# Kernel optimization log

Hardware: AMD Instinct MI355X
Metric: run time of the kernel (lower is better)

## Reference

```python
import jax, jax.numpy as jnp
import numpy as np
import math

D_MODEL = 512
N_HEAD = 8
D_FF = 2048
B, S, S_ENC = 2, 2048, 2048
EPS = 1e-5


def _linear_params(key, d_in, d_out):
    kw, kb = jax.random.split(key)
    w = jax.random.normal(kw, (d_in, d_out), dtype=jnp.float32) * 0.02
    b = jax.random.normal(kb, (d_out,), dtype=jnp.float32) * 0.02
    return w, b


def setup_inputs() -> dict:
    key = jax.random.key(0)
    ks = jax.random.split(key, 16)
    dec = jax.random.normal(ks[0], (B, S, D_MODEL), dtype=jnp.float32)
    enc = jax.random.normal(ks[1], (B, S_ENC, D_MODEL), dtype=jnp.float32)
    src_mask = jnp.ones((B, 1, 1, S_ENC), dtype=jnp.int32)  # no padding
    tgt_mask = jnp.tril(jnp.ones((S, S), dtype=jnp.int32))[None, None]  # causal
    inp = {"dec": dec, "enc": enc, "src_mask": src_mask, "tgt_mask": tgt_mask}
    # self-attention projections
    for i, nm in enumerate(["sa_wq", "sa_wk", "sa_wv", "sa_wo"]):
        w, b = _linear_params(ks[2 + i], D_MODEL, D_MODEL)
        inp[nm], inp[nm.replace("w", "b")] = w, b
    # cross-attention projections
    for i, nm in enumerate(["ca_wq", "ca_wk", "ca_wv", "ca_wo"]):
        w, b = _linear_params(ks[6 + i], D_MODEL, D_MODEL)
        inp[nm], inp[nm.replace("w", "b")] = w, b
    # FFN
    inp["ffn_w1"], inp["ffn_b1"] = _linear_params(ks[10], D_MODEL, D_FF)
    inp["ffn_w2"], inp["ffn_b2"] = _linear_params(ks[11], D_FF, D_MODEL)
    # LayerNorms (gamma=1, beta=0 init as in torch)
    for i in (1, 2, 3):
        inp[f"ln{i}_g"] = jnp.ones((D_MODEL,), dtype=jnp.float32)
        inp[f"ln{i}_b"] = jnp.zeros((D_MODEL,), dtype=jnp.float32)
    return inp


def _layer_norm(x, g, b):
    mu = jnp.mean(x, axis=-1, keepdims=True)
    var = jnp.mean(jnp.square(x - mu), axis=-1, keepdims=True)
    return (x - mu) * jax.lax.rsqrt(var + EPS) * g + b


def _mha(xq, xkv, wq, bq, wk, bk, wv, bv, wo, bo, mask):
    Bq, Sq, D = xq.shape
    Sk = xkv.shape[1]
    d_k = D // N_HEAD
    def split(x, s):
        return x.reshape(x.shape[0], s, N_HEAD, d_k).transpose(0, 2, 1, 3)  # [B,H,S,dk]
    q = split(xq @ wq + bq, Sq)
    k = split(xkv @ wk + bk, Sk)
    v = split(xkv @ wv + bv, Sk)
    scores = jnp.einsum("bhqd,bhkd->bhqk", q, k) / math.sqrt(d_k)
    if mask is not None:
        scores = jnp.where(mask == 0, jnp.float32(-1e9), scores)
    attn = jax.nn.softmax(scores, axis=-1)
    out = jnp.einsum("bhqk,bhkd->bhqd", attn, v)
    out = out.transpose(0, 2, 1, 3).reshape(Bq, Sq, D)
    return out @ wo + bo


def reference(dec, enc, src_mask, tgt_mask,
              sa_wq, sa_bq, sa_wk, sa_bk, sa_wv, sa_bv, sa_wo, sa_bo,
              ca_wq, ca_bq, ca_wk, ca_bk, ca_wv, ca_bv, ca_wo, ca_bo,
              ffn_w1, ffn_b1, ffn_w2, ffn_b2,
              ln1_g, ln1_b, ln2_g, ln2_b, ln3_g, ln3_b):
    # dropout is identity in eval mode
    x = _mha(dec, dec, sa_wq, sa_bq, sa_wk, sa_bk, sa_wv, sa_bv, sa_wo, sa_bo, tgt_mask)
    x = _layer_norm(x + dec, ln1_g, ln1_b)
    _x = x
    x = _mha(x, enc, ca_wq, ca_bq, ca_wk, ca_bk, ca_wv, ca_bv, ca_wo, ca_bo, src_mask)
    x = _layer_norm(x + _x, ln2_g, ln2_b)
    _x = x
    x = jax.nn.relu(x @ ffn_w1 + ffn_b1) @ ffn_w2 + ffn_b2
    x = _layer_norm(x + _x, ln3_g, ln3_b)
    return x
```

## Files before the change

### kernel.cpp

```cpp
#include <hip/hip_runtime.h>


#define D_MODEL 512
#define NHEAD 8
#define DK 64
#define SEQ 2048
#define MTOK 4096
#define DFF 2048

typedef __attribute__((ext_vector_type(8))) short bf16x8;
typedef __attribute__((ext_vector_type(4))) float f32x4;

__device__ __forceinline__ unsigned short f2bf(float x) {
  unsigned u = __float_as_uint(x);
  u += 0x7FFF + ((u >> 16) & 1);
  return (unsigned short)(u >> 16);
}
__device__ __forceinline__ unsigned pack2(float a, float b) {
  return (unsigned)f2bf(a) | ((unsigned)f2bf(b) << 16);
}
__device__ __forceinline__ void load_lds16(const unsigned short* g, unsigned short* l) {
  __builtin_amdgcn_global_load_lds(
      (const __attribute__((address_space(1))) void*)g,
      (__attribute__((address_space(3))) void*)l, 16, 0, 0);
}

struct WDesc { const float* src; unsigned short* dst; int K; int N; };
struct WPack { WDesc d[10]; };

__global__ __launch_bounds__(256)
void wprep_kernel(WPack p) {
  const WDesc wd = p.d[blockIdx.y];
  const int ntx = wd.N >> 5;
  const int ntile = (wd.K >> 5) * ntx;
  if ((int)blockIdx.x >= ntile) return;
  const int n0 = (blockIdx.x % ntx) * 32;
  const int k0 = (blockIdx.x / ntx) * 32;
  __shared__ float T[32][33];
  const int tid = threadIdx.x;
  {
    const int r = tid >> 3, c4 = (tid & 7) * 4;
    float4 v = *(const float4*)(wd.src + (long)(k0 + r) * wd.N + n0 + c4);
    T[r][c4] = v.x; T[r][c4 + 1] = v.y; T[r][c4 + 2] = v.z; T[r][c4 + 3] = v.w;
  }
  __syncthreads();
  {
    const int n = tid >> 3, kq = (tid & 7) * 4;
    ushort4 o;
    o.x = f2bf(T[kq + 0][n]); o.y = f2bf(T[kq + 1][n]);
    o.z = f2bf(T[kq + 2][n]); o.w = f2bf(T[kq + 3][n]);
    *(ushort4*)(wd.dst + (long)(n0 + n) * wd.K + k0 + kq) = o;
  }
}

__global__ __launch_bounds__(256)
void cast_kernel(const float* __restrict__ s, unsigned short* __restrict__ d, int n8) {
  const int i = blockIdx.x * 256 + threadIdx.x;
  if (i >= n8) return;
  float4 a = *(const float4*)(s + (long)i * 8);
  float4 b = *(const float4*)(s + (long)i * 8 + 4);
  uint4 o;
  o.x = pack2(a.x, a.y); o.y = pack2(a.z, a.w);
  o.z = pack2(b.x, b.y); o.w = pack2(b.z, b.w);
  *(uint4*)(d + (long)i * 8) = o;
}

template<int MODE>
__global__ __launch_bounds__(256)
void gemm_bf16(const unsigned short* __restrict__ A, const unsigned short* __restrict__ Wt,
               const float* __restrict__ bias, const float* __restrict__ res,
               void* __restrict__ outp, int M, int N, int K, float scale) {
  __shared__ unsigned short As[4096];
  __shared__ unsigned short Bs[2048];
  const int tid = threadIdx.x;
  const int w = tid >> 6, lane = tid & 63, g = lane >> 4, li = lane & 15;
  const int m0 = blockIdx.x * 128, n0 = blockIdx.y * 64;
  const int wm = w >> 1, wn = w & 1;

  f32x4 acc[4][2] = {};
  const int a0kg = tid >> 7, a0m = tid & 127;
  const int a1kg = (tid + 256) >> 7, a1m = (tid + 256) & 127;
  const int bkg = tid >> 6, bn = tid & 63;
  const unsigned short* Ap0 = A + (long)(m0 + a0m) * K + a0kg * 8;
  const unsigned short* Ap1 = A + (long)(m0 + a1m) * K + a1kg * 8;
  const unsigned short* Bp = Wt + (long)(n0 + bn) * K + bkg * 8;

  for (int k0 = 0; k0 < K; k0 += 32) {
    __syncthreads();
    load_lds16(Ap0 + k0, &As[(w * 64) * 8]);
    load_lds16(Ap1 + k0, &As[(256 + w * 64) * 8]);
    load_lds16(Bp + k0, &Bs[(w * 64) * 8]);
    __syncthreads();
    bf16x8 af[4], bfr[2];
#pragma unroll
    for (int mf = 0; mf < 4; mf++)
      af[mf] = *(const bf16x8*)&As[(g * 128 + wm * 64 + mf * 16 + li) * 8];
#pragma unroll
    for (int nf = 0; nf < 2; nf++)
      bfr[nf] = *(const bf16x8*)&Bs[(g * 64 + wn * 32 + nf * 16 + li) * 8];
#pragma unroll
    for (int mf = 0; mf < 4; mf++)
#pragma unroll
      for (int nf = 0; nf < 2; nf++)
        acc[mf][nf] = __builtin_amdgcn_mfma_f32_16x16x32_bf16(af[mf], bfr[nf], acc[mf][nf], 0, 0, 0);
  }

#pragma unroll
  for (int nf = 0; nf < 2; nf++) {
    const int c = n0 + wn * 32 + nf * 16 + li;
    const float bv = bias[c];
#pragma unroll
    for (int mf = 0; mf < 4; mf++) {
#pragma unroll
      for (int j = 0; j < 4; j++) {
        const int r = m0 + wm * 64 + mf * 16 + g * 4 + j;
        float v = acc[mf][nf][j] + bv;
        if (MODE == 0) {
          v *= scale;
          const int b = r >> 11, s = r & (SEQ - 1), h = c >> 6, d = c & 63;
          ((unsigned short*)outp)[(((long)(b * NHEAD + h)) * SEQ + s) * DK + d] = f2bf(v);
        } else if (MODE == 1) {
          v += res[(long)r * N + c];
          ((float*)outp)[(long)r * N + c] = v;
        } else {
          v = fmaxf(v, 0.f);
          ((unsigned short*)outp)[(long)r * N + c] = f2bf(v);
        }
      }
    }
  }
}

template<bool CAUSAL>
__global__ __launch_bounds__(256)
void attn_bf16(const unsigned short* __restrict__ Qg, const unsigned short* __restrict__ Kg,
               const unsigned short* __restrict__ Vg, unsigned short* __restrict__ Og) {
  __shared__ unsigned short Qp[8192];
  __shared__ unsigned short Kp[4096];
  __shared__ unsigned short Vt[4096];
  __shared__ unsigned short Pl[4][2048];
  const int tid = threadIdx.x;
  const int w = tid >> 6, lane = tid & 63, g = lane >> 4, li = lane & 15;
  const int qb = blockIdx.x, bh = blockIdx.y;
  const int q0 = qb * 128;
  const long base = (long)bh * SEQ * DK;

#pragma unroll
  for (int i = 0; i < 4; i++) {
    const int idx = i * 256 + tid;
    const int dg = idx >> 7, q = idx & 127;
    load_lds16(Qg + base + (long)(q0 + q) * DK + dg * 8, &Qp[(i * 256 + w * 64) * 8]);
  }
  __syncthreads();
  bf16x8 bq[2][2];
#pragma unroll
  for (int qf = 0; qf < 2; qf++)
#pragma unroll
    for (int ks = 0; ks < 2; ks++)
      bq[qf][ks] = *(const bf16x8*)&Qp[((ks * 4 + g) * 128 + w * 32 + qf * 16 + li) * 8];

  f32x4 oacc[2][4] = {};
  float mrun[2] = {-1e30f, -1e30f};
  float denom[2] = {0.f, 0.f};

  const int vdg = tid >> 5;
  const int vs0 = (tid & 31) * 2;
  const int vsg = vs0 >> 3, vso = vs0 & 7;

  const int ntile = CAUSAL ? (2 * qb + 2) : (SEQ / 64);
  for (int t = 0; t < ntile; t++) {
    const int k0 = t * 64;
    __syncthreads();
#pragma unroll
    for (int i = 0; i < 2; i++) {
      const int idx = i * 256 + tid;
      const int dg = idx >> 6, kk = idx & 63;
      load_lds16(Kg + base + (long)(k0 + kk) * DK + dg * 8, &Kp[(i * 256 + w * 64) * 8]);
    }
    {
      const unsigned short* vsrc = Vg + base + (long)(k0 + vs0) * DK + vdg * 8;
      uint4 r0 = *(const uint4*)vsrc;
      uint4 r1 = *(const uint4*)(vsrc + DK);
      unsigned short u0[8], u1[8];
      *(uint4*)u0 = r0; *(uint4*)u1 = r1;
#pragma unroll
      for (int e = 0; e < 8; e++) {
        const int d = vdg * 8 + e;
        const int dsw = d ^ (vsg & 7);
        *(unsigned*)&Vt[(vsg * 64 + dsw) * 8 + vso] =
            (unsigned)u0[e] | ((unsigned)u1[e] << 16);
      }
    }
    __syncthreads();

    f32x4 sacc[4][2] = {};
#pragma unroll
    for (int ks = 0; ks < 2; ks++) {
#pragma unroll
      for (int kf = 0; kf < 4; kf++) {
        bf16x8 ka = *(const bf16x8*)&Kp[((ks * 4 + g) * 64 + kf * 16 + li) * 8];
#pragma unroll
        for (int qf = 0; qf < 2; qf++)
          sacc[kf][qf] = __builtin_amdgcn_mfma_f32_16x16x32_bf16(ka, bq[qf][ks], sacc[kf][qf], 0, 0, 0);
      }
    }
    if (CAUSAL && t >= 2 * qb) {
#pragma unroll
      for (int kf = 0; kf < 4; kf++)
#pragma unroll
        for (int qf = 0; qf < 2; qf++)
#pragma unroll
          for (int j = 0; j < 4; j++) {
            const int kg_ = k0 + kf * 16 + g * 4 + j;
            const int qg_ = q0 + w * 32 + qf * 16 + li;
            if (kg_ > qg_) sacc[kf][qf][j] = -1e30f;
          }
    }
    float corrv[2];
#pragma unroll
    for (int qf = 0; qf < 2; qf++) {
      float mx = -1e30f;
#pragma unroll
      for (int kf = 0; kf < 4; kf++)
#pragma unroll
        for (int j = 0; j < 4; j++) mx = fmaxf(mx, sacc[kf][qf][j]);
      mx = fmaxf(mx, __shfl_xor(mx, 16, 64));
      mx = fmaxf(mx, __shfl_xor(mx, 32, 64));
      const float mn = fmaxf(mrun[qf], mx);
      const float corr = __expf(mrun[qf] - mn);
      mrun[qf] = mn;
      float ps = 0.f;
#pragma unroll
      for (int kf = 0; kf < 4; kf++)
#pragma unroll
        for (int j = 0; j < 4; j++) {
          const float p = __expf(sacc[kf][qf][j] - mn);
          sacc[kf][qf][j] = p;
          ps += p;
        }
      ps += __shfl_xor(ps, 16, 64);
      ps += __shfl_xor(ps, 32, 64);
      denom[qf] = denom[qf] * corr + ps;
      corrv[qf] = corr;
    }
#pragma unroll
    for (int mf = 0; mf < 2; mf++)
#pragma unroll
      for (int j = 0; j < 4; j++) {
        const float cf = __shfl(corrv[mf], g * 4 + j, 64);
#pragma unroll
        for (int df = 0; df < 4; df++) oacc[mf][df][j] *= cf;
      }
#pragma unroll
    for (int kf = 0; kf < 4; kf++)
#pragma unroll
      for (int qf = 0; qf < 2; qf++) {
        uint2 pv;
        pv.x = pack2(sacc[kf][qf][0], sacc[kf][qf][1]);
        pv.y = pack2(sacc[kf][qf][2], sacc[kf][qf][3]);
        *(uint2*)&Pl[w][((kf * 2 + (g >> 1)) * 32 + qf * 16 + li) * 8 + (g & 1) * 4] = pv;
      }
#pragma unroll
    for (int ks2 = 0; ks2 < 2; ks2++) {
      const int sg = ks2 * 4 + g;
#pragma unroll
      for (int mf = 0; mf < 2; mf++) {
        bf16x8 pa = *(const bf16x8*)&Pl[w][(sg * 32 + mf * 16 + li) * 8];
#pragma unroll
        for (int df = 0; df < 4; df++) {
          bf16x8 vb = *(const bf16x8*)&Vt[(sg * 64 + ((df * 16 + li) ^ (sg & 7))) * 8];
          oacc[mf][df] = __builtin_amdgcn_mfma_f32_16x16x32_bf16(pa, vb, oacc[mf][df], 0, 0, 0);
        }
      }
    }
  }

  const int b = bh >> 3, h = bh & 7;
  float rinv[2] = {1.f / denom[0], 1.f / denom[1]};
#pragma unroll
  for (int mf = 0; mf < 2; mf++)
#pragma unroll
    for (int j = 0; j < 4; j++) {
      const float dj = __shfl(rinv[mf], g * 4 + j, 64);
      const int q = q0 + w * 32 + mf * 16 + g * 4 + j;
#pragma unroll
      for (int df = 0; df < 4; df++) {
        const int col = h * DK + df * 16 + li;
        Og[((long)(b * SEQ + q)) * D_MODEL + col] = f2bf(oacc[mf][df][j] * dj);
      }
    }
}

template<bool DUAL>
__global__ __launch_bounds__(256)
void ln_kernel(const float* __restrict__ x, const float* __restrict__ gam,
               const float* __restrict__ bet, float* __restrict__ out,
               unsigned short* __restrict__ outb) {
  const int row = blockIdx.x * 4 + (threadIdx.x >> 6);
  const int lane = threadIdx.x & 63;
  const float* xr = x + (long)row * D_MODEL;
  float4 v0 = *(const float4*)&xr[lane * 8];
  float4 v1 = *(const float4*)&xr[lane * 8 + 4];
  float xv[8] = {v0.x, v0.y, v0.z, v0.w, v1.x, v1.y, v1.z, v1.w};
  float s = 0.f, s2 = 0.f;
#pragma unroll
  for (int i = 0; i < 8; i++) { s += xv[i]; s2 = fmaf(xv[i], xv[i], s2); }
#pragma unroll
  for (int off = 32; off > 0; off >>= 1) {
    s += __shfl_xor(s, off, 64);
    s2 += __shfl_xor(s2, off, 64);
  }
  const float mu = s * (1.f / D_MODEL);
  const float var = fmaxf(s2 * (1.f / D_MODEL) - mu * mu, 0.f);
  const float rstd = rsqrtf(var + 1e-5f);
  float y[8];
#pragma unroll
  for (int i = 0; i < 8; i++) {
    const int c = lane * 8 + i;
    y[i] = (xv[i] - mu) * rstd * gam[c] + bet[c];
  }
  float* orow = out + (long)row * D_MODEL + lane * 8;
  *(float4*)orow = make_float4(y[0], y[1], y[2], y[3]);
  *(float4*)(orow + 4) = make_float4(y[4], y[5], y[6], y[7]);
  if (DUAL) {
    uint4 o;
    o.x = pack2(y[0], y[1]); o.y = pack2(y[2], y[3]);
    o.z = pack2(y[4], y[5]); o.w = pack2(y[6], y[7]);
    *(uint4*)(outb + (long)row * D_MODEL + lane * 8) = o;
  }
}

extern "C" void kernel_launch(void* const* d_in, const int* in_sizes, int n_in,
                              void* d_out, int out_size, void* d_ws, size_t ws_size,
                              hipStream_t stream) {
  const float* dec = (const float*)d_in[0];
  const float* enc = (const float*)d_in[1];
  const float* sa_wq = (const float*)d_in[4];
  const float* sa_bq = (const float*)d_in[5];
  const float* sa_wk = (const float*)d_in[6];
  const float* sa_bk = (const float*)d_in[7];
  const float* sa_wv = (const float*)d_in[8];
  const float* sa_bv = (const float*)d_in[9];
  const float* sa_wo = (const float*)d_in[10];
  const float* sa_bo = (const float*)d_in[11];
  const float* ca_wq = (const float*)d_in[12];
  const float* ca_bq = (const float*)d_in[13];
  const float* ca_wk = (const float*)d_in[14];
  const float* ca_bk = (const float*)d_in[15];
  const float* ca_wv = (const float*)d_in[16];
  const float* ca_bv = (const float*)d_in[17];
  const float* ca_wo = (const float*)d_in[18];
  const float* ca_bo = (const float*)d_in[19];
  const float* ffn_w1 = (const float*)d_in[20];
  const float* ffn_b1 = (const float*)d_in[21];
  const float* ffn_w2 = (const float*)d_in[22];
  const float* ffn_b2 = (const float*)d_in[23];
  const float* ln1_g = (const float*)d_in[24];
  const float* ln1_b = (const float*)d_in[25];
  const float* ln2_g = (const float*)d_in[26];
  const float* ln2_b = (const float*)d_in[27];
  const float* ln3_g = (const float*)d_in[28];
  const float* ln3_b = (const float*)d_in[29];

  unsigned short* U = (unsigned short*)d_ws;
  unsigned short* wq_t = U + 0;
  unsigned short* wk_t = U + 262144;
  unsigned short* wv_t = U + 524288;
  unsigned short* wo_t = U + 786432;
  unsigned short* cq_t = U + 1048576;
  unsigned short* ck_t = U + 1310720;
  unsigned short* cv_t = U + 1572864;
  unsigned short* co_t = U + 1835008;
  unsigned short* f1_t = U + 2097152;
  unsigned short* f2_t = U + 3145728;
  unsigned short* dec_bf = U + 4194304;
  unsigned short* enc_bf = U + 6291456;
  unsigned short* Qb  = U + 8388608;
  unsigned short* Kb  = U + 10485760;
  unsigned short* Vb  = U + 12582912;
  unsigned short* AOb = U + 14680064;
  unsigned short* X1b = U + 16777216;
  unsigned short* X2b = U + 18874368;
  unsigned short* MIDb = U + 20971520;
  float* F = (float*)(U + 29360128);
  float* R  = F;
  float* X1 = F + 2097152;
  float* X2 = F + 4194304;

  dim3 blk(256);
  dim3 g512(MTOK / 128, D_MODEL / 64);
  dim3 gff1(MTOK / 128, DFF / 64);
  dim3 gattn(SEQ / 128, 2 * NHEAD);

  WPack wp;
  wp.d[0] = {sa_wq, wq_t, D_MODEL, D_MODEL};
  wp.d[1] = {sa_wk, wk_t, D_MODEL, D_MODEL};
  wp.d[2] = {sa_wv, wv_t, D_MODEL, D_MODEL};
  wp.d[3] = {sa_wo, wo_t, D_MODEL, D_MODEL};
  wp.d[4] = {ca_wq, cq_t, D_MODEL, D_MODEL};
  wp.d[5] = {ca_wk, ck_t, D_MODEL, D_MODEL};
  wp.d[6] = {ca_wv, cv_t, D_MODEL, D_MODEL};
  wp.d[7] = {ca_wo, co_t, D_MODEL, D_MODEL};
  wp.d[8] = {ffn_w1, f1_t, D_MODEL, DFF};
  wp.d[9] = {ffn_w2, f2_t, DFF, D_MODEL};
  wprep_kernel<<<dim3(1024, 10), blk, 0, stream>>>(wp);
  cast_kernel<<<1024, blk, 0, stream>>>(dec, dec_bf, MTOK * D_MODEL / 8);
  cast_kernel<<<1024, blk, 0, stream>>>(enc, enc_bf, MTOK * D_MODEL / 8);

  gemm_bf16<0><<<g512, blk, 0, stream>>>(dec_bf, wq_t, sa_bq, nullptr, Qb, MTOK, D_MODEL, D_MODEL, 0.125f);
  gemm_bf16<0><<<g512, blk, 0, stream>>>(dec_bf, wk_t, sa_bk, nullptr, Kb, MTOK, D_MODEL, D_MODEL, 1.f);
  gemm_bf16<0><<<g512, blk, 0, stream>>>(dec_bf, wv_t, sa_bv, nullptr, Vb, MTOK, D_MODEL, D_MODEL, 1.f);
  attn_bf16<true><<<gattn, blk, 0, stream>>>(Qb, Kb, Vb, AOb);
  gemm_bf16<1><<<g512, blk, 0, stream>>>(AOb, wo_t, sa_bo, dec, R, MTOK, D_MODEL, D_MODEL, 1.f);
  ln_kernel<true><<<MTOK / 4, blk, 0, stream>>>(R, ln1_g, ln1_b, X1, X1b);

  gemm_bf16<0><<<g512, blk, 0, stream>>>(X1b, cq_t, ca_bq, nullptr, Qb, MTOK, D_MODEL, D_MODEL, 0.125f);
  gemm_bf16<0><<<g512, blk, 0, stream>>>(enc_bf, ck_t, ca_bk, nullptr, Kb, MTOK, D_MODEL, D_MODEL, 1.f);
  gemm_bf16<0><<<g512, blk, 0, stream>>>(enc_bf, cv_t, ca_bv, nullptr, Vb, MTOK, D_MODEL, D_MODEL, 1.f);
  attn_bf16<false><<<gattn, blk, 0, stream>>>(Qb, Kb, Vb, AOb);
  gemm_bf16<1><<<g512, blk, 0, stream>>>(AOb, co_t, ca_bo, X1, R, MTOK, D_MODEL, D_MODEL, 1.f);
  ln_kernel<true><<<MTOK / 4, blk, 0, stream>>>(R, ln2_g, ln2_b, X2, X2b);

  gemm_bf16<2><<<gff1, blk, 0, stream>>>(X2b, f1_t, ffn_b1, nullptr, MIDb, MTOK, DFF, D_MODEL, 1.f);
  gemm_bf16<1><<<g512, blk, 0, stream>>>(MIDb, f2_t, ffn_b2, X2, R, MTOK, D_MODEL, DFF, 1.f);
  ln_kernel<false><<<MTOK / 4, blk, 0, stream>>>(R, ln3_g, ln3_b, (float*)d_out, nullptr);
}
```

Before: 500.8 us.

## Fuse QKV GEMMs, split-K attention with combine, recompute LN residuals in epilogue

Concatenates the Q/K/V (and cross K/V) weight matrices so each projection set runs as one GEMM, and adds a BM=64 tile variant for the N=512 GEMMs to raise block count. Attention is split into four KV chunks along a new grid dimension, with partial outputs and stats combined by a separate kernel, and softmax now uses exp2 with log2e folded into the Q scale. LayerNorm no longer writes an fp32 copy; later residual GEMMs rebuild it from saved mean and rstd. This trades extra partial-output traffic and a combine launch for more parallelism and fewer launches and copies.

```diff
diff --git a/kernel.cpp b/kernel.cpp
--- a/kernel.cpp
+++ b/kernel.cpp
@@ -65,41 +65,52 @@
   *(uint4*)(d + (long)i * 8) = o;
 }
 
-template<int MODE>
+template<int MODE, int BM>
 __global__ __launch_bounds__(256)
 void gemm_bf16(const unsigned short* __restrict__ A, const unsigned short* __restrict__ Wt,
-               const float* __restrict__ bias, const float* __restrict__ res,
-               void* __restrict__ outp, int M, int N, int K, float scale) {
-  __shared__ unsigned short As[4096];
+               const float* __restrict__ b0, const float* __restrict__ b1,
+               const float* __restrict__ b2, const float* res,
+               const float* __restrict__ lnm, const float* __restrict__ lnr,
+               const float* __restrict__ lng, const float* __restrict__ lnbt,
+               unsigned short* __restrict__ o0, unsigned short* __restrict__ o1,
+               unsigned short* __restrict__ o2, float* of,
+               int M, int N, int K, float scale0) {
+  constexpr int MF = BM / 32;
+  __shared__ unsigned short As[BM * 32];
   __shared__ unsigned short Bs[2048];
   const int tid = threadIdx.x;
   const int w = tid >> 6, lane = tid & 63, g = lane >> 4, li = lane & 15;
-  const int m0 = blockIdx.x * 128, n0 = blockIdx.y * 64;
+  const int m0 = blockIdx.x * BM, n0 = blockIdx.y * 64;
   const int wm = w >> 1, wn = w & 1;
 
-  f32x4 acc[4][2] = {};
-  const int a0kg = tid >> 7, a0m = tid & 127;
-  const int a1kg = (tid + 256) >> 7, a1m = (tid + 256) & 127;
+  f32x4 acc[MF][2] = {};
   const int bkg = tid >> 6, bn = tid & 63;
-  const unsigned short* Ap0 = A + (long)(m0 + a0m) * K + a0kg * 8;
-  const unsigned short* Ap1 = A + (long)(m0 + a1m) * K + a1kg * 8;
   const unsigned short* Bp = Wt + (long)(n0 + bn) * K + bkg * 8;
+
+  const unsigned short* Ap0;
+  const unsigned short* Ap1 = nullptr;
+  if constexpr (BM == 128) {
+    Ap0 = A + (long)(m0 + (tid & 127)) * K + (tid >> 7) * 8;
+    Ap1 = A + (long)(m0 + (tid & 127)) * K + ((tid >> 7) + 2) * 8;
+  } else {
+    Ap0 = A + (long)(m0 + (tid & 63)) * K + (tid >> 6) * 8;
+  }
 
   for (int k0 = 0; k0 < K; k0 += 32) {
     __syncthreads();
     load_lds16(Ap0 + k0, &As[(w * 64) * 8]);
-    load_lds16(Ap1 + k0, &As[(256 + w * 64) * 8]);
+    if constexpr (BM == 128) load_lds16(Ap1 + k0, &As[(256 + w * 64) * 8]);
     load_lds16(Bp + k0, &Bs[(w * 64) * 8]);
     __syncthreads();
-    bf16x8 af[4], bfr[2];
-#pragma unroll
-    for (int mf = 0; mf < 4; mf++)
-      af[mf] = *(const bf16x8*)&As[(g * 128 + wm * 64 + mf * 16 + li) * 8];
+    bf16x8 af[MF], bfr[2];
+#pragma unroll
+    for (int mf = 0; mf < MF; mf++)
+      af[mf] = *(const bf16x8*)&As[(g * BM + wm * (BM / 2) + mf * 16 + li) * 8];
 #pragma unroll
     for (int nf = 0; nf < 2; nf++)
       bfr[nf] = *(const bf16x8*)&Bs[(g * 64 + wn * 32 + nf * 16 + li) * 8];
 #pragma unroll
-    for (int mf = 0; mf < 4; mf++)
+    for (int mf = 0; mf < MF; mf++)
 #pragma unroll
       for (int nf = 0; nf < 2; nf++)
         acc[mf][nf] = __builtin_amdgcn_mfma_f32_16x16x32_bf16(af[mf], bfr[nf], acc[mf][nf], 0, 0, 0);
@@ -108,23 +119,37 @@
 #pragma unroll
   for (int nf = 0; nf < 2; nf++) {
     const int c = n0 + wn * 32 + nf * 16 + li;
-    const float bv = bias[c];
-#pragma unroll
-    for (int mf = 0; mf < 4; mf++) {
+    float bias, scl = 1.f;
+    unsigned short* hdst = nullptr;
+    float lngv = 0.f, lnbv = 0.f;
+    if constexpr (MODE == 0) {
+      const int which = c >> 9;
+      bias = (which == 0 ? b0 : (which == 1 ? b1 : b2))[c & 511];
+      if (which == 0) scl = scale0;
+      hdst = which == 0 ? o0 : (which == 1 ? o1 : o2);
+    } else {
+      bias = b0[c];
+      if constexpr (MODE == 3) { lngv = lng[c]; lnbv = lnbt[c]; }
+    }
+#pragma unroll
+    for (int mf = 0; mf < MF; mf++) {
 #pragma unroll
       for (int j = 0; j < 4; j++) {
-        const int r = m0 + wm * 64 + mf * 16 + g * 4 + j;
-        float v = acc[mf][nf][j] + bv;
-        if (MODE == 0) {
-          v *= scale;
-          const int b = r >> 11, s = r & (SEQ - 1), h = c >> 6, d = c & 63;
-          ((unsigned short*)outp)[(((long)(b * NHEAD + h)) * SEQ + s) * DK + d] = f2bf(v);
-        } else if (MODE == 1) {
+        const int r = m0 + wm * (BM / 2) + mf * 16 + g * 4 + j;
+        float v = acc[mf][nf][j] + bias;
+        if constexpr (MODE == 0) {
+          v *= scl;
+          const int b = r >> 11, s = r & (SEQ - 1), h = (c >> 6) & 7, d = c & 63;
+          hdst[(((long)(b * NHEAD + h)) * SEQ + s) * DK + d] = f2bf(v);
+        } else if constexpr (MODE == 1) {
           v += res[(long)r * N + c];
-          ((float*)outp)[(long)r * N + c] = v;
+          of[(long)r * N + c] = v;
+        } else if constexpr (MODE == 2) {
+          o0[(long)r * N + c] = f2bf(fmaxf(v, 0.f));
         } else {
-          v = fmaxf(v, 0.f);
-          ((unsigned short*)outp)[(long)r * N + c] = f2bf(v);
+          const float xr = res[(long)r * N + c];
+          v += (xr - lnm[r]) * lnr[r] * lngv + lnbv;
+          of[(long)r * N + c] = v;
         }
       }
     }
@@ -134,16 +159,18 @@
 template<bool CAUSAL>
 __global__ __launch_bounds__(256)
 void attn_bf16(const unsigned short* __restrict__ Qg, const unsigned short* __restrict__ Kg,
-               const unsigned short* __restrict__ Vg, unsigned short* __restrict__ Og) {
-  __shared__ unsigned short Qp[8192];
-  __shared__ unsigned short Kp[4096];
-  __shared__ unsigned short Vt[4096];
-  __shared__ unsigned short Pl[4][2048];
+               const unsigned short* __restrict__ Vg, float* __restrict__ Opart,
+               float* __restrict__ Mst, float* __restrict__ Lst) {
+  __shared__ unsigned short SM[16384];
+  unsigned short* const Qp = SM;
+  unsigned short* const Kp = SM + 8192;
+  unsigned short* const Vt = SM + 12288;
   const int tid = threadIdx.x;
   const int w = tid >> 6, lane = tid & 63, g = lane >> 4, li = lane & 15;
-  const int qb = blockIdx.x, bh = blockIdx.y;
+  const int qb = blockIdx.x, bh = blockIdx.y, ck = blockIdx.z;
   const int q0 = qb * 128;
   const long base = (long)bh * SEQ * DK;
+  unsigned short* const Pl = SM + w * 2048;
 
 #pragma unroll
   for (int i = 0; i < 4; i++) {
@@ -167,8 +194,10 @@
   const int vs0 = (tid & 31) * 2;
   const int vsg = vs0 >> 3, vso = vs0 & 7;
 
-  const int ntile = CAUSAL ? (2 * qb + 2) : (SEQ / 64);
-  for (int t = 0; t < ntile; t++) {
+  const int tbeg = CAUSAL ? ck : ck * 8;
+  const int tend = CAUSAL ? (2 * qb + 2) : (ck * 8 + 8);
+  const int tstep = CAUSAL ? 4 : 1;
+  for (int t = tbeg; t < tend; t += tstep) {
     const int k0 = t * 64;
     __syncthreads();
 #pragma unroll
@@ -227,14 +256,14 @@
       mx = fmaxf(mx, __shfl_xor(mx, 16, 64));
       mx = fmaxf(mx, __shfl_xor(mx, 32, 64));
       const float mn = fmaxf(mrun[qf], mx);
-      const float corr = __expf(mrun[qf] - mn);
+      const float corr = exp2f(mrun[qf] - mn);
       mrun[qf] = mn;
       float ps = 0.f;
 #pragma unroll
       for (int kf = 0; kf < 4; kf++)
 #pragma unroll
         for (int j = 0; j < 4; j++) {
-          const float p = __expf(sacc[kf][qf][j] - mn);
+          const float p = exp2f(sacc[kf][qf][j] - mn);
           sacc[kf][qf][j] = p;
           ps += p;
         }
@@ -258,14 +287,14 @@
         uint2 pv;
         pv.x = pack2(sacc[kf][qf][0], sacc[kf][qf][1]);
         pv.y = pack2(sacc[kf][qf][2], sacc[kf][qf][3]);
-        *(uint2*)&Pl[w][((kf * 2 + (g >> 1)) * 32 + qf * 16 + li) * 8 + (g & 1) * 4] = pv;
+        *(uint2*)&Pl[((kf * 2 + (g >> 1)) * 32 + qf * 16 + li) * 8 + (g & 1) * 4] = pv;
       }
 #pragma unroll
     for (int ks2 = 0; ks2 < 2; ks2++) {
       const int sg = ks2 * 4 + g;
 #pragma unroll
       for (int mf = 0; mf < 2; mf++) {
-        bf16x8 pa = *(const bf16x8*)&Pl[w][(sg * 32 + mf * 16 + li) * 8];
+        bf16x8 pa = *(const bf16x8*)&Pl[(sg * 32 + mf * 16 + li) * 8];
 #pragma unroll
         for (int df = 0; df < 4; df++) {
           bf16x8 vb = *(const bf16x8*)&Vt[(sg * 64 + ((df * 16 + li) ^ (sg & 7))) * 8];
@@ -275,27 +304,56 @@
     }
   }
 
+  const long pbase = (long)(ck * 16 + bh) * SEQ;
+  if (g == 0) {
+#pragma unroll
+    for (int qf = 0; qf < 2; qf++) {
+      const int q = q0 + w * 32 + qf * 16 + li;
+      Mst[pbase + q] = mrun[qf];
+      Lst[pbase + q] = denom[qf];
+    }
+  }
+#pragma unroll
+  for (int mf = 0; mf < 2; mf++)
+#pragma unroll
+    for (int j = 0; j < 4; j++) {
+      const int q = q0 + w * 32 + mf * 16 + g * 4 + j;
+      float* op = Opart + (pbase + q) * 64;
+#pragma unroll
+      for (int df = 0; df < 4; df++) op[df * 16 + li] = oacc[mf][df][j];
+    }
+}
+
+__global__ __launch_bounds__(256)
+void combine_kernel(const float* __restrict__ Opart, const float* __restrict__ Mst,
+                    const float* __restrict__ Lst, unsigned short* __restrict__ AOb) {
+  const int row = blockIdx.x * 4 + (threadIdx.x >> 6);
+  const int lane = threadIdx.x & 63;
+  const int bh = row >> 11, q = row & (SEQ - 1);
+  float m[4], l[4], mstar = -1e30f;
+#pragma unroll
+  for (int c = 0; c < 4; c++) {
+    m[c] = Mst[((long)c * 16 + bh) * SEQ + q];
+    l[c] = Lst[((long)c * 16 + bh) * SEQ + q];
+    mstar = fmaxf(mstar, m[c]);
+  }
+  float den = 0.f, o = 0.f;
+#pragma unroll
+  for (int c = 0; c < 4; c++) {
+    const float wgt = exp2f(m[c] - mstar);
+    den += wgt * l[c];
+    o += wgt * Opart[(((long)c * 16 + bh) * SEQ + q) * 64 + lane];
+  }
   const int b = bh >> 3, h = bh & 7;
-  float rinv[2] = {1.f / denom[0], 1.f / denom[1]};
-#pragma unroll
-  for (int mf = 0; mf < 2; mf++)
-#pragma unroll
-    for (int j = 0; j < 4; j++) {
-      const float dj = __shfl(rinv[mf], g * 4 + j, 64);
-      const int q = q0 + w * 32 + mf * 16 + g * 4 + j;
-#pragma unroll
-      for (int df = 0; df < 4; df++) {
-        const int col = h * DK + df * 16 + li;
-        Og[((long)(b * SEQ + q)) * D_MODEL + col] = f2bf(oacc[mf][df][j] * dj);
-      }
-    }
-}
-
-template<bool DUAL>
+  AOb[((long)(b * SEQ + q)) * D_MODEL + h * DK + lane] = f2bf(o / den);
+}
+
+template<int V>
 __global__ __launch_bounds__(256)
 void ln_kernel(const float* __restrict__ x, const float* __restrict__ gam,
-               const float* __restrict__ bet, float* __restrict__ out,
-               unsigned short* __restrict__ outb) {
+               const float* __restrict__ bet, float* __restrict__ outf,
+               unsigned short* __restrict__ outb, float* __restrict__ mu_s,
+               float* __restrict__ rs_s) {
   const int row = blockIdx.x * 4 + (threadIdx.x >> 6);
   const int lane = threadIdx.x & 63;
   const float* xr = x + (long)row * D_MODEL;
@@ -319,14 +377,16 @@
     const int c = lane * 8 + i;
     y[i] = (xv[i] - mu) * rstd * gam[c] + bet[c];
   }
-  float* orow = out + (long)row * D_MODEL + lane * 8;
-  *(float4*)orow = make_float4(y[0], y[1], y[2], y[3]);
-  *(float4*)(orow + 4) = make_float4(y[4], y[5], y[6], y[7]);
-  if (DUAL) {
+  if constexpr (V == 0) {
     uint4 o;
     o.x = pack2(y[0], y[1]); o.y = pack2(y[2], y[3]);
     o.z = pack2(y[4], y[5]); o.w = pack2(y[6], y[7]);
     *(uint4*)(outb + (long)row * D_MODEL + lane * 8) = o;
+    if (lane == 0) { mu_s[row] = mu; rs_s[row] = rstd; }
+  } else {
+    float* orow = outf + (long)row * D_MODEL + lane * 8;
+    *(float4*)orow = make_float4(y[0], y[1], y[2], y[3]);
+    *(float4*)(orow + 4) = make_float4(y[4], y[5], y[6], y[7]);
   }
 }
 
@@ -362,66 +422,72 @@
   const float* ln3_g = (const float*)d_in[28];
   const float* ln3_b = (const float*)d_in[29];
 
-  unsigned short* U = (unsigned short*)d_ws;
-  unsigned short* wq_t = U + 0;
-  unsigned short* wk_t = U + 262144;
-  unsigned short* wv_t = U + 524288;
-  unsigned short* wo_t = U + 786432;
-  unsigned short* cq_t = U + 1048576;
-  unsigned short* ck_t = U + 1310720;
-  unsigned short* cv_t = U + 1572864;
-  unsigned short* co_t = U + 1835008;
-  unsigned short* f1_t = U + 2097152;
-  unsigned short* f2_t = U + 3145728;
-  unsigned short* dec_bf = U + 4194304;
-  unsigned short* enc_bf = U + 6291456;
-  unsigned short* Qb  = U + 8388608;
-  unsigned short* Kb  = U + 10485760;
-  unsigned short* Vb  = U + 12582912;
-  unsigned short* AOb = U + 14680064;
-  unsigned short* X1b = U + 16777216;
-  unsigned short* X2b = U + 18874368;
-  unsigned short* MIDb = U + 20971520;
-  float* F = (float*)(U + 29360128);
-  float* R  = F;
-  float* X1 = F + 2097152;
-  float* X2 = F + 4194304;
+  char* wsb = (char*)d_ws;
+  unsigned short* dec_bf = (unsigned short*)wsb;
+  float* Opart = (float*)wsb;
+  float* Mst = (float*)(wsb + 33554432);
+  float* Lst = (float*)(wsb + 34078720);
+  unsigned short* MIDb = (unsigned short*)wsb;
+  size_t off = 34603008;
+  unsigned short* qkv_t = (unsigned short*)(wsb + off); off += 1572864;
+  unsigned short* wo_t  = (unsigned short*)(wsb + off); off += 524288;
+  unsigned short* cq_t  = (unsigned short*)(wsb + off); off += 524288;
+  unsigned short* ckv_t = (unsigned short*)(wsb + off); off += 1048576;
+  unsigned short* co_t  = (unsigned short*)(wsb + off); off += 524288;
+  unsigned short* f1_t  = (unsigned short*)(wsb + off); off += 2097152;
+  unsigned short* f2_t  = (unsigned short*)(wsb + off); off += 2097152;
+  unsigned short* enc_bf = (unsigned short*)(wsb + off); off += 4194304;
+  unsigned short* Qb  = (unsigned short*)(wsb + off); off += 4194304;
+  unsigned short* Kb  = (unsigned short*)(wsb + off); off += 4194304;
+  unsigned short* Vb  = (unsigned short*)(wsb + off); off += 4194304;
+  unsigned short* AOb = (unsigned short*)(wsb + off); off += 4194304;
+  unsigned short* X1b = (unsigned short*)(wsb + off); off += 4194304;
+  unsigned short* X2b = (unsigned short*)(wsb + off); off += 4194304;
+  float* R   = (float*)(wsb + off); off += 8388608;
+  float* mu1 = (float*)(wsb + off); off += 16384;
+  float* rs1 = (float*)(wsb + off); off += 16384;
+  float* mu2 = (float*)(wsb + off); off += 16384;
+  float* rs2 = (float*)(wsb + off); off += 16384;
 
   dim3 blk(256);
-  dim3 g512(MTOK / 128, D_MODEL / 64);
-  dim3 gff1(MTOK / 128, DFF / 64);
-  dim3 gattn(SEQ / 128, 2 * NHEAD);
+  const float QS = 0.125f * 1.44269504f;
 
   WPack wp;
-  wp.d[0] = {sa_wq, wq_t, D_MODEL, D_MODEL};
-  wp.d[1] = {sa_wk, wk_t, D_MODEL, D_MODEL};
-  wp.d[2] = {sa_wv, wv_t, D_MODEL, D_MODEL};
-  wp.d[3] = {sa_wo, wo_t, D_MODEL, D_MODEL};
-  wp.d[4] = {ca_wq, cq_t, D_MODEL, D_MODEL};
-  wp.d[5] = {ca_wk, ck_t, D_MODEL, D_MODEL};
-  wp.d[6] = {ca_wv, cv_t, D_MODEL, D_MODEL};
-  wp.d[7] = {ca_wo, co_t, D_MODEL, D_MODEL};
-  wp.d[8] = {ffn_w1, f1_t, D_MODEL, DFF};
-  wp.d[9] = {ffn_w2, f2_t, DFF, D_MODEL};
+  wp.d[0] = {sa_wq, qkv_t, 512, 512};
+  wp.d[1] = {sa_wk, qkv_t + 262144, 512, 512};
+  wp.d[2] = {sa_wv, qkv_t + 524288, 512, 512};
+  wp.d[3] = {sa_wo, wo_t, 512, 512};
+  wp.d[4] = {ca_wq, cq_t, 512, 512};
+  wp.d[5] = {ca_wk, ckv_t, 512, 512};
+  wp.d[6] = {ca_wv, ckv_t + 262144, 512, 512};
+  wp.d[7] = {ca_wo, co_t, 512, 512};
+  wp.d[8] = {ffn_w1, f1_t, 512, 2048};
+  wp.d[9] = {ffn_w2, f2_t, 2048, 512};
   wprep_kernel<<<dim3(1024, 10), blk, 0, stream>>>(wp);
-  cast_kernel<<<1024, blk, 0, stream>>>(dec, dec_bf, MTOK * D_MODEL / 8);
-  cast_kernel<<<1024, blk, 0, stream>>>(enc, enc_bf, MTOK * D_MODEL / 8);
-
-  gemm_bf16<0><<<g512, blk, 0, stream>>>(dec_bf, wq_t, sa_bq, nullptr, Qb, MTOK, D_MODEL, D_MODEL, 0.125f);
-  gemm_bf16<0><<<g512, blk, 0, stream>>>(dec_bf, wk_t, sa_bk, nullptr, Kb, MTOK, D_MODEL, D_MODEL, 1.f);
-  gemm_bf16<0><<<g512, blk, 0, stream>>>(dec_bf, wv_t, sa_bv, nullptr, Vb, MTOK, D_MODEL, D_MODEL, 1.f);
-  attn_bf16<true><<<gattn, blk, 0, stream>>>(Qb, Kb, Vb, AOb);
-  gemm_bf16<1><<<g512, blk, 0, stream>>>(AOb, wo_t, sa_bo, dec, R, MTOK, D_MODEL, D_MODEL, 1.f);
-  ln_kernel<true><<<MTOK / 4, blk, 0, stream>>>(R, ln1_g, ln1_b, X1, X1b);
-
-  gemm_bf16<0><<<g512, blk, 0, stream>>>(X1b, cq_t, ca_bq, nullptr, Qb, MTOK, D_MODEL, D_MODEL, 0.125f);
-  gemm_bf16<0><<<g512, blk, 0, stream>>>(enc_bf, ck_t, ca_bk, nullptr, Kb, MTOK, D_MODEL, D_MODEL, 1.f);
-  gemm_bf16<0><<<g512, blk, 0, stream>>>(enc_bf, cv_t, ca_bv, nullptr, Vb, MTOK, D_MODEL, D_MODEL, 1.f);
-  attn_bf16<false><<<gattn, blk, 0, stream>>>(Qb, Kb, Vb, AOb);
-  gemm_bf16<1><<<g512, blk, 0, stream>>>(AOb, co_t, ca_bo, X1, R, MTOK, D_MODEL, D_MODEL, 1.f);
-  ln_kernel<true><<<MTOK / 4, blk, 0, stream>>>(R, ln2_g, ln2_b, X2, X2b);
-
-  gemm_bf16<2><<<gff1, blk, 0, stream>>>(X2b, f1_t, ffn_b1, nullptr, MIDb, MTOK, DFF, D_MODEL, 1.f);
-  gemm_bf16<1><<<g512, blk, 0, stream>>>(MIDb, f2_t, ffn_b2, X2, R, MTOK, D_MODEL, DFF, 1.f);
-  ln_kernel<false><<<MTOK / 4, blk, 0, stream>>>(R, ln3_g, ln3_b, (float*)d_out, nullptr);
-}
+  cast_kernel<<<1024, blk, 0, stream>>>(dec, dec_bf, 262144);
+  cast_kernel<<<1024, blk, 0, stream>>>(enc, enc_bf, 262144);
+
+  gemm_bf16<0, 128><<<dim3(32, 24), blk, 0, stream>>>(dec_bf, qkv_t, sa_bq, sa_bk, sa_bv,
+      nullptr, nullptr, nullptr, nullptr, nullptr, Qb, Kb, Vb, nullptr, MTOK, 1536, 512, QS);
+  attn_bf16<true><<<dim3(16, 16, 4), blk, 0, stream>>>(Qb, Kb, Vb, Opart, Mst, Lst);
+  combine_kernel<<<8192, blk, 0, stream>>>(Opart, Mst, Lst, AOb);
+  gemm_bf16<1, 64><<<dim3(64, 8), blk, 0, stream>>>(AOb, wo_t, sa_bo, nullptr, nullptr,
+      dec, nullptr, nullptr, nullptr, nullptr, nullptr, nullptr, nullptr, R, MTOK, 512, 512, 1.f);
+  ln_kernel<0><<<1024, blk, 0, stream>>>(R, ln1_g, ln1_b, nullptr, X1b, mu1, rs1);
+
+  gemm_bf16<0, 64><<<dim3(64, 8), blk, 0, stream>>>(X1b, cq_t, ca_bq, nullptr, nullptr,
+      nullptr, nullptr, nullptr, nullptr, nullptr, Qb, nullptr, nullptr, nullptr, MTOK, 512, 512, QS);
+  gemm_bf16<0, 128><<<dim3(32, 16), blk, 0, stream>>>(enc_bf, ckv_t, ca_bk, ca_bv, nullptr,
+      nullptr, nullptr, nullptr, nullptr, nullptr, Kb, Vb, nullptr, nullptr, MTOK, 1024, 512, 1.f);
+  attn_bf16<false><<<dim3(16, 16, 4), blk, 0, stream>>>(Qb, Kb, Vb, Opart, Mst, Lst);
+  combine_kernel<<<8192, blk, 0, stream>>>(Opart, Mst, Lst, AOb);
+  gemm_bf16<3, 64><<<dim3(64, 8), blk, 0, stream>>>(AOb, co_t, ca_bo, nullptr, nullptr,
+      R, mu1, rs1, ln1_g, ln1_b, nullptr, nullptr, nullptr, R, MTOK, 512, 512, 1.f);
+  ln_kernel<0><<<1024, blk, 0, stream>>>(R, ln2_g, ln2_b, nullptr, X2b, mu2, rs2);
+
+  gemm_bf16<2, 128><<<dim3(32, 32), blk, 0, stream>>>(X2b, f1_t, ffn_b1, nullptr, nullptr,
+      nullptr, nullptr, nullptr, nullptr, nullptr, MIDb, nullptr, nullptr, nullptr, MTOK, 2048, 512, 1.f);
+  gemm_bf16<3, 64><<<dim3(64, 8), blk, 0, stream>>>(MIDb, f2_t, ffn_b2, nullptr, nullptr,
+      R, mu2, rs2, ln2_g, ln2_b, nullptr, nullptr, nullptr, R, MTOK, 512, 2048, 1.f);
+  ln_kernel<1><<<1024, blk, 0, stream>>>(R, ln3_g, ln3_b, (float*)d_out, nullptr, nullptr, nullptr);
+}
```

New measurement: 435.0 us. 13.1% less time.
